# Optimization experiments

Hardware: AMD Instinct MI355X
Metric: run time of the kernel (lower is better)

The kernel has to match this reference:

```python
import jax, jax.numpy as jnp
import numpy as np

T, C, H = 4096, 1024, 16
D = C // H  # head dim = 64


def setup_inputs() -> dict:
    key = jax.random.key(0)
    k1, k2, k3 = jax.random.split(key, 3)
    x = jax.random.normal(k1, (T, C), dtype=jnp.float32)
    w_attn = jax.random.normal(k2, (C, 3 * C), dtype=jnp.float32) * (1.0 / np.sqrt(C))
    w_proj = jax.random.normal(k3, (C, C), dtype=jnp.float32) * (1.0 / np.sqrt(C))
    return {"x": x, "w_attn": w_attn, "w_proj": w_proj, "num_frames": 64}


def reference(x, w_attn, w_proj, num_frames):
    t, c = x.shape
    d = c // H
    qkv = x @ w_attn                       # (T, 3C)
    q, k, v = jnp.split(qkv, 3, axis=-1)   # each (T, C)
    # (T, H, D) -> (H, T, D)
    q = q.reshape(t, H, d).transpose(1, 0, 2)
    k = k.reshape(t, H, d).transpose(1, 0, 2)
    v = v.reshape(t, H, d).transpose(1, 0, 2)
    # causal mask with dense global prefix: every query may attend to the
    # first num_frames keys in addition to the causal lower triangle.
    rows = jnp.arange(t)[:, None]
    cols = jnp.arange(t)[None, :]
    mask = (cols <= rows) | (cols < num_frames)   # (T, T) bool
    scores = jnp.einsum('htd,hsd->hts', q, k) * (1.0 / np.sqrt(d))  # (H,T,T)
    scores = jnp.where(mask[None], scores, jnp.float32(-jnp.inf))
    att = jax.nn.softmax(scores, axis=-1)
    y = jnp.einsum('hts,hsd->htd', att, v)        # (H, T, D)
    y = y.transpose(1, 0, 2).reshape(t, c)        # (T, C)
    return y @ w_proj
```

## Files before the change

kernel.cpp:

```cpp
#include <hip/hip_runtime.h>
#include <hip/hip_bf16.h>

#define Tq 4096
#define Cdim 1024
#define NH 16
#define DH 64

typedef __attribute__((ext_vector_type(8))) short short8;
typedef __attribute__((ext_vector_type(4))) float f32x4;

#define SCLQ 0.1803368801111204f

__device__ __forceinline__ unsigned short f2bf(float f) {
  union { float f; unsigned int u; } v; v.f = f;
  unsigned int r = v.u + 0x7FFFu + ((v.u >> 16) & 1u);
  return (unsigned short)(r >> 16);
}

__device__ __forceinline__ float bf2f(unsigned short u) {
  union { unsigned int u; float f; } v; v.u = ((unsigned int)u) << 16;
  return v.f;
}

__device__ __forceinline__ unsigned int cvtpk_bf16(float lo, float hi) {
  unsigned int r;
  asm volatile("v_cvt_pk_bf16_f32 %0, %1, %2" : "=v"(r) : "v"(lo), "v"(hi));
  return r;
}

__global__ void cvt_kernel(const float* __restrict__ in, unsigned short* __restrict__ out, int n) {
  int idx = (blockIdx.x * blockDim.x + threadIdx.x) * 4;
  if (idx + 3 < n) {
    float4 v = *reinterpret_cast<const float4*>(in + idx);
    ushort4 o;
    o.x = f2bf(v.x); o.y = f2bf(v.y); o.z = f2bf(v.z); o.w = f2bf(v.w);
    *reinterpret_cast<ushort4*>(out + idx) = o;
  }
}

__global__ void transpose_cvt(const float* __restrict__ in, unsigned short* __restrict__ out,
                              int R, int Ccols) {
  __shared__ float tile[64][65];
  int c0 = blockIdx.x * 64, r0 = blockIdx.y * 64;
  int tx = threadIdx.x & 63;
  int ty = threadIdx.x >> 6;
  #pragma unroll
  for (int rr = 0; rr < 64; rr += 4)
    tile[rr + ty][tx] = in[(r0 + rr + ty) * Ccols + c0 + tx];
  __syncthreads();
  #pragma unroll
  for (int rr = 0; rr < 64; rr += 4)
    out[(c0 + rr + ty) * R + r0 + tx] = f2bf(tile[tx][rr + ty]);
}

template<int OUT_MODE>
__global__ __launch_bounds__(256, 3)
void gemm_bt(const unsigned short* __restrict__ A,
             const unsigned short* __restrict__ B,
             void* __restrict__ Cout,
             int M, int N, int K)
{
  __shared__ __align__(16) unsigned short As[128][64];
  __shared__ __align__(16) unsigned short Bs[128][64];
  const int tid = threadIdx.x;
  const int lane = tid & 63;
  const int wave = tid >> 6;
  const int wm = wave >> 1, wn = wave & 1;

  const int chunk = gridDim.x >> 3;
  const int b = blockIdx.x;
  const int swz = (b & 7) * chunk + (b >> 3);
  const int n0 = (swz >> 5) * 128;
  const int m0 = (swz & 31) * 128;

  f32x4 acc[4][4] = {};

  const int lrow = lane >> 3;
  const int lcol = (lane & 7) * 8;

  for (int k0 = 0; k0 < K; k0 += 64) {
    __syncthreads();
    #pragma unroll
    for (int t = 0; t < 4; ++t) {
      const int r = wave * 32 + t * 8;
      __builtin_amdgcn_global_load_lds(
        (const __attribute__((address_space(1))) void*)&A[(size_t)(m0 + r + lrow) * K + k0 + lcol],
        (__attribute__((address_space(3))) void*)&As[r][0], 16, 0, 0);
      __builtin_amdgcn_global_load_lds(
        (const __attribute__((address_space(1))) void*)&B[(size_t)(n0 + r + lrow) * K + k0 + lcol],
        (__attribute__((address_space(3))) void*)&Bs[r][0], 16, 0, 0);
    }
    __syncthreads();
    #pragma unroll
    for (int kk = 0; kk < 64; kk += 32) {
      const int frow = lane & 15;
      const int fcol = kk + 8 * (lane >> 4);
      short8 a[4], bfr[4];
      #pragma unroll
      for (int i = 0; i < 4; ++i) {
        a[i]   = *reinterpret_cast<const short8*>(&As[wm * 64 + i * 16 + frow][fcol]);
        bfr[i] = *reinterpret_cast<const short8*>(&Bs[wn * 64 + i * 16 + frow][fcol]);
      }
      #pragma unroll
      for (int i = 0; i < 4; ++i)
        #pragma unroll
        for (int j = 0; j < 4; ++j)
          acc[i][j] = __builtin_amdgcn_mfma_f32_16x16x32_bf16(a[i], bfr[j], acc[i][j], 0, 0, 0);
    }
  }

  const int rbase = (lane >> 4) * 4;
  const int ccol = lane & 15;
  #pragma unroll
  for (int i = 0; i < 4; ++i) {
    const int row0 = m0 + wm * 64 + i * 16 + rbase;
    #pragma unroll
    for (int j = 0; j < 4; ++j) {
      const int col = n0 + wn * 64 + j * 16 + ccol;
      if (OUT_MODE == 0) {
        unsigned short* q = (unsigned short*)Cout;
        int sec = col >> 10, rem = col & 1023;
        int hh = rem >> 6, d = rem & 63;
        if (sec == 2) {
          ushort4 pk;
          pk.x = f2bf(acc[i][j][0]); pk.y = f2bf(acc[i][j][1]);
          pk.z = f2bf(acc[i][j][2]); pk.w = f2bf(acc[i][j][3]);
          *reinterpret_cast<ushort4*>(
              &q[((size_t)(2 * NH + hh) * DH + d) * Tq + row0]) = pk;
        } else {
          const float mult = (sec == 0) ? SCLQ : 1.0f;
          #pragma unroll
          for (int r = 0; r < 4; ++r)
            q[(((size_t)sec * NH + hh) * Tq + row0 + r) * DH + d] = f2bf(acc[i][j][r] * mult);
        }
      } else {
        #pragma unroll
        for (int r = 0; r < 4; ++r)
          ((float*)Cout)[(row0 + r) * N + col] = acc[i][j][r];
      }
    }
  }
}

__global__ __launch_bounds__(256, 4)
void attn_kernel(const unsigned short* __restrict__ qkv,
                 unsigned short* __restrict__ po01,
                 unsigned short* __restrict__ po2,
                 float* __restrict__ pl,
                 const int* __restrict__ nf_ptr)
{
  __shared__ __align__(16) unsigned short Ks[128][72];
  __shared__ __align__(16) unsigned short VTs[64][136];

  const int tid  = threadIdx.x;
  const int lane = tid & 63;
  const int w    = tid >> 6;
  const int g    = lane >> 4;
  const int li   = lane & 15;

  const int h   = blockIdx.x & 15;
  const int bb  = blockIdx.x >> 4;
  const int s   = bb % 3;
  const int qc  = 63 - bb / 3;
  const int q0  = qc * 64;
  const int nf  = nf_ptr[0];

  const unsigned short* Qh  = qkv + (size_t)h * Tq * DH;
  const unsigned short* Kh  = qkv + (size_t)(NH + h) * Tq * DH;
  const unsigned short* VTh = qkv + (size_t)(2 * NH + h) * DH * Tq;

  const int qrow = q0 + w * 16 + li;
  short8 qf[2];
  #pragma unroll
  for (int kk = 0; kk < 2; ++kk)
    qf[kk] = *reinterpret_cast<const short8*>(&Qh[qrow * DH + kk * 32 + 8 * g]);

  f32x4 o[4] = {};
  f32x4 ol = {};

  short8 ones;
  #pragma unroll
  for (int e = 0; e < 8; ++e) ones[e] = (short)0x3F80;

  int lastt = q0 + 63;
  if (nf - 1 > lastt) lastt = nf - 1;
  const int T = (lastt >> 7) + 1;

  const int krow0 = tid >> 3;
  const int kcol  = (tid & 7) * 8;
  const int vrow0 = tid >> 4;
  const int vcol  = (tid & 15) * 8;

  {
    const int nx = s * 128;
    short8 nk[4], nv[4];
    #pragma unroll
    for (int j = 0; j < 4; ++j) {
      nk[j] = *reinterpret_cast<const short8*>(&Kh[(nx + krow0 + 32 * j) * DH + kcol]);
      nv[j] = *reinterpret_cast<const short8*>(&VTh[(size_t)(vrow0 + 16 * j) * Tq + nx + vcol]);
    }
    #pragma unroll
    for (int j = 0; j < 4; ++j) {
      *reinterpret_cast<short8*>(&Ks[krow0 + 32 * j][kcol]) = nk[j];
      *reinterpret_cast<short8*>(&VTs[vrow0 + 16 * j][vcol]) = nv[j];
    }
  }
  __syncthreads();

  for (int t = s; t < T; t += 3) {
    const int kv0 = t * 128;
    const bool havenext = (t + 3 < T);
    short8 nk[4], nv[4];
    if (havenext) {
      const int nx = kv0 + 384;
      #pragma unroll
      for (int j = 0; j < 4; ++j) {
        nk[j] = *reinterpret_cast<const short8*>(&Kh[(nx + krow0 + 32 * j) * DH + kcol]);
        nv[j] = *reinterpret_cast<const short8*>(&VTh[(size_t)(vrow0 + 16 * j) * Tq + nx + vcol]);
      }
    }

    #pragma unroll
    for (int h2 = 0; h2 < 2; ++h2) {
      const int kvb = kv0 + h2 * 64;

      f32x4 sarr[4];
      __builtin_amdgcn_s_setprio(1);
      #pragma unroll
      for (int nb = 0; nb < 4; ++nb) {
        f32x4 a = {};
        #pragma unroll
        for (int kk = 0; kk < 2; ++kk) {
          short8 kf = *reinterpret_cast<const short8*>(
              &Ks[h2 * 64 + nb * 16 + li][kk * 32 + 8 * g]);
          a = __builtin_amdgcn_mfma_f32_16x16x32_bf16(kf, qf[kk], a, 0, 0, 0);
        }
        sarr[nb] = a;
      }
      __builtin_amdgcn_s_setprio(0);

      const bool needmask = !((kvb + 63 <= q0 + w * 16) || (kvb + 63 < nf));
      float p[4][4];
      #pragma unroll
      for (int nb = 0; nb < 4; ++nb) {
        #pragma unroll
        for (int r = 0; r < 4; ++r) {
          float v = sarr[nb][r];
          if (needmask) {
            const int kvi = kvb + nb * 16 + 4 * g + r;
            if (!(kvi <= qrow || kvi < nf)) v = -1e30f;
          }
          p[nb][r] = exp2f(v);
        }
      }

      #pragma unroll
      for (int kk = 0; kk < 2; ++kk) {
        unsigned int X1 = cvtpk_bf16(p[2 * kk][0], p[2 * kk][1]);
        unsigned int X2 = cvtpk_bf16(p[2 * kk][2], p[2 * kk][3]);
        unsigned int Y1 = cvtpk_bf16(p[2 * kk + 1][0], p[2 * kk + 1][1]);
        unsigned int Y2 = cvtpk_bf16(p[2 * kk + 1][2], p[2 * kk + 1][3]);
        asm volatile("v_permlane32_swap_b32 %0, %1" : "+v"(X1), "+v"(Y1));
        asm volatile("v_permlane32_swap_b32 %0, %1" : "+v"(X2), "+v"(Y2));
        asm volatile("v_permlane16_swap_b32 %0, %1" : "+v"(X1), "+v"(Y1));
        asm volatile("v_permlane16_swap_b32 %0, %1" : "+v"(X2), "+v"(Y2));
        union { unsigned int u[4]; short8 s8; } W;
        W.u[0] = X1; W.u[1] = X2; W.u[2] = Y1; W.u[3] = Y2;
        __builtin_amdgcn_s_setprio(1);
        #pragma unroll
        for (int db = 0; db < 4; ++db) {
          short8 vb = *reinterpret_cast<const short8*>(
              &VTs[db * 16 + li][h2 * 64 + kk * 32 + 8 * g]);
          o[db] = __builtin_amdgcn_mfma_f32_16x16x32_bf16(vb, W.s8, o[db], 0, 0, 0);
        }
        ol = __builtin_amdgcn_mfma_f32_16x16x32_bf16(ones, W.s8, ol, 0, 0, 0);
        __builtin_amdgcn_s_setprio(0);
      }
    }

    if (havenext) {
      __syncthreads();
      #pragma unroll
      for (int j = 0; j < 4; ++j) {
        *reinterpret_cast<short8*>(&Ks[krow0 + 32 * j][kcol]) = nk[j];
        *reinterpret_cast<short8*>(&VTs[vrow0 + 16 * j][vcol]) = nv[j];
      }
      __syncthreads();
    }
  }

  unsigned short* pp = (s == 2 ? po2 : po01 + (size_t)s * NH * Tq * DH)
                       + ((size_t)h * Tq + qrow) * DH;
  #pragma unroll
  for (int db = 0; db < 4; ++db) {
    ushort4 pk;
    pk.x = f2bf(o[db][0]);
    pk.y = f2bf(o[db][1]);
    pk.z = f2bf(o[db][2]);
    pk.w = f2bf(o[db][3]);
    *reinterpret_cast<ushort4*>(&pp[db * 16 + 4 * g]) = pk;
  }
  if (g == 0)
    pl[((size_t)s * NH + h) * Tq + qrow] = ol[0];
}

__global__ __launch_bounds__(256)
void merge_kernel(const unsigned short* __restrict__ po01,
                  const unsigned short* __restrict__ po2,
                  const float* __restrict__ pl,
                  unsigned short* __restrict__ ybf)
{
  const int idx = blockIdx.x * 256 + threadIdx.x;
  const int d8  = idx & 7;
  const int row = (idx >> 3) & 4095;
  const int h   = idx >> 15;
  const size_t base = ((size_t)h * Tq + row) * DH + d8 * 8;
  short8 a = *reinterpret_cast<const short8*>(&po01[base]);
  short8 b = *reinterpret_cast<const short8*>(&po01[(size_t)NH * Tq * DH + base]);
  short8 c = *reinterpret_cast<const short8*>(&po2[base]);
  const float l0 = pl[(size_t)h * Tq + row];
  const float l1 = pl[((size_t)NH + h) * Tq + row];
  const float l2 = pl[((size_t)2 * NH + h) * Tq + row];
  const float inv = 1.0f / (l0 + l1 + l2);
  short8 outv;
  #pragma unroll
  for (int j = 0; j < 8; ++j) {
    float v = (bf2f((unsigned short)a[j]) + bf2f((unsigned short)b[j])
               + bf2f((unsigned short)c[j])) * inv;
    outv[j] = (short)f2bf(v);
  }
  *reinterpret_cast<short8*>(&ybf[(size_t)row * Cdim + h * DH + d8 * 8]) = outv;
}

extern "C" void kernel_launch(void* const* d_in, const int* in_sizes, int n_in,
                              void* d_out, int out_size, void* d_ws, size_t ws_size,
                              hipStream_t stream) {
  (void)in_sizes; (void)n_in; (void)out_size; (void)ws_size;
  const float* x  = (const float*)d_in[0];
  const float* wa = (const float*)d_in[1];
  const float* wp = (const float*)d_in[2];
  const int*   nf = (const int*)d_in[3];
  float* out = (float*)d_out;

  char* ws = (char*)d_ws;
  unsigned short* x_bf = (unsigned short*)(ws);
  unsigned short* waT  = (unsigned short*)(ws + (size_t)8  * 1024 * 1024);
  unsigned short* wpT  = (unsigned short*)(ws + (size_t)14 * 1024 * 1024);
  unsigned short* qkvb = (unsigned short*)(ws + (size_t)16 * 1024 * 1024);
  unsigned short* ybf  = (unsigned short*)(ws + (size_t)40 * 1024 * 1024);

  unsigned short* po01 = (unsigned short*)d_out;
  float* pl = (float*)(ws);
  unsigned short* po2 = (unsigned short*)(ws + (size_t)1 * 1024 * 1024);

  cvt_kernel<<<4096, 256, 0, stream>>>(x, x_bf, Tq * Cdim);
  transpose_cvt<<<dim3(48, 16), 256, 0, stream>>>(wa, waT, 1024, 3072);
  transpose_cvt<<<dim3(16, 16), 256, 0, stream>>>(wp, wpT, 1024, 1024);
  gemm_bt<0><<<768, 256, 0, stream>>>(x_bf, waT, (void*)qkvb, Tq, 3 * Cdim, Cdim);
  attn_kernel<<<3072, 256, 0, stream>>>(qkvb, po01, po2, pl, nf);
  merge_kernel<<<2048, 256, 0, stream>>>(po01, po2, pl, ybf);
  gemm_bt<1><<<256, 256, 0, stream>>>(ybf, wpT, (void*)out, Tq, Cdim, Cdim);
}
```

Baseline: 150.0 us.

## Load K/V MFMA fragments directly from global memory, dropping LDS staging

The attention kernel no longer stages K and V^T tiles through shared memory with a register prefetch and double barrier. Each wave now loads its MFMA operand fragments straight from global memory (relying on L1/L2 to share them across the 4 waves) and keeps only a lightweight s_barrier per iteration to keep waves roughly in step. This removes LDS traffic and __syncthreads stalls, but each wave issues its own redundant global loads and the software prefetch of the next tile is gone, so load latency may be exposed.

```diff
diff --git a/kernel.cpp b/kernel.cpp
--- a/kernel.cpp
+++ b/kernel.cpp
@@ -149,9 +149,6 @@
                  float* __restrict__ pl,
                  const int* __restrict__ nf_ptr)
 {
-  __shared__ __align__(16) unsigned short Ks[128][72];
-  __shared__ __align__(16) unsigned short VTs[64][136];
-
   const int tid  = threadIdx.x;
   const int lane = tid & 63;
   const int w    = tid >> 6;
@@ -186,43 +183,29 @@
   if (nf - 1 > lastt) lastt = nf - 1;
   const int T = (lastt >> 7) + 1;
 
-  const int krow0 = tid >> 3;
-  const int kcol  = (tid & 7) * 8;
-  const int vrow0 = tid >> 4;
-  const int vcol  = (tid & 15) * 8;
-
-  {
-    const int nx = s * 128;
-    short8 nk[4], nv[4];
-    #pragma unroll
-    for (int j = 0; j < 4; ++j) {
-      nk[j] = *reinterpret_cast<const short8*>(&Kh[(nx + krow0 + 32 * j) * DH + kcol]);
-      nv[j] = *reinterpret_cast<const short8*>(&VTh[(size_t)(vrow0 + 16 * j) * Tq + nx + vcol]);
-    }
-    #pragma unroll
-    for (int j = 0; j < 4; ++j) {
-      *reinterpret_cast<short8*>(&Ks[krow0 + 32 * j][kcol]) = nk[j];
-      *reinterpret_cast<short8*>(&VTs[vrow0 + 16 * j][vcol]) = nv[j];
-    }
-  }
-  __syncthreads();
+  const int kfo = li * DH + 8 * g;
+  const size_t vfo = (size_t)li * Tq + 8 * g;
 
   for (int t = s; t < T; t += 3) {
     const int kv0 = t * 128;
-    const bool havenext = (t + 3 < T);
-    short8 nk[4], nv[4];
-    if (havenext) {
-      const int nx = kv0 + 384;
-      #pragma unroll
-      for (int j = 0; j < 4; ++j) {
-        nk[j] = *reinterpret_cast<const short8*>(&Kh[(nx + krow0 + 32 * j) * DH + kcol]);
-        nv[j] = *reinterpret_cast<const short8*>(&VTh[(size_t)(vrow0 + 16 * j) * Tq + nx + vcol]);
-      }
-    }
 
     #pragma unroll
     for (int h2 = 0; h2 < 2; ++h2) {
       const int kvb = kv0 + h2 * 64;
+      const unsigned short* kb = Kh + (size_t)kvb * DH + kfo;
+      const unsigned short* vbp = VTh + vfo + kvb;
+
+      short8 kf[4][2], vv[4][2];
+      #pragma unroll
+      for (int nb = 0; nb < 4; ++nb)
+        #pragma unroll
+        for (int kk = 0; kk < 2; ++kk)
+          kf[nb][kk] = *reinterpret_cast<const short8*>(&kb[nb * 16 * DH + kk * 32]);
+      #pragma unroll
+      for (int db = 0; db < 4; ++db)
+        #pragma unroll
+        for (int kk = 0; kk < 2; ++kk)
+          vv[db][kk] = *reinterpret_cast<const short8*>(&vbp[(size_t)db * 16 * Tq + kk * 32]);
 
       f32x4 sarr[4];
       __builtin_amdgcn_s_setprio(1);
@@ -230,11 +213,8 @@
       for (int nb = 0; nb < 4; ++nb) {
         f32x4 a = {};
         #pragma unroll
-        for (int kk = 0; kk < 2; ++kk) {
-          short8 kf = *reinterpret_cast<const short8*>(
-              &Ks[h2 * 64 + nb * 16 + li][kk * 32 + 8 * g]);
-          a = __builtin_amdgcn_mfma_f32_16x16x32_bf16(kf, qf[kk], a, 0, 0, 0);
-        }
+        for (int kk = 0; kk < 2; ++kk)
+          a = __builtin_amdgcn_mfma_f32_16x16x32_bf16(kf[nb][kk], qf[kk], a, 0, 0, 0);
         sarr[nb] = a;
       }
       __builtin_amdgcn_s_setprio(0);
@@ -268,25 +248,14 @@
         W.u[0] = X1; W.u[1] = X2; W.u[2] = Y1; W.u[3] = Y2;
         __builtin_amdgcn_s_setprio(1);
         #pragma unroll
-        for (int db = 0; db < 4; ++db) {
-          short8 vb = *reinterpret_cast<const short8*>(
-              &VTs[db * 16 + li][h2 * 64 + kk * 32 + 8 * g]);
-          o[db] = __builtin_amdgcn_mfma_f32_16x16x32_bf16(vb, W.s8, o[db], 0, 0, 0);
-        }
+        for (int db = 0; db < 4; ++db)
+          o[db] = __builtin_amdgcn_mfma_f32_16x16x32_bf16(vv[db][kk], W.s8, o[db], 0, 0, 0);
         ol = __builtin_amdgcn_mfma_f32_16x16x32_bf16(ones, W.s8, ol, 0, 0, 0);
         __builtin_amdgcn_s_setprio(0);
       }
     }
 
-    if (havenext) {
-      __syncthreads();
-      #pragma unroll
-      for (int j = 0; j < 4; ++j) {
-        *reinterpret_cast<short8*>(&Ks[krow0 + 32 * j][kcol]) = nk[j];
-        *reinterpret_cast<short8*>(&VTs[vrow0 + 16 * j][vcol]) = nv[j];
-      }
-      __syncthreads();
-    }
+    __builtin_amdgcn_s_barrier();
   }
 
   unsigned short* pp = (s == 2 ? po2 : po01 + (size_t)s * NH * Tq * DH)
```

Result: slower. 326.7 us (+117.7%).

## Process 128 query rows per attention block, reusing K/V fragments across two row tiles

Applied to the files above, without the earlier changes.

Each attention workgroup now covers 128 query rows instead of 64, and each wave handles two 16-row sub-tiles. K fragments are loaded from LDS once and reused for both sub-tiles, and V fragments are shared across both PV MFMAs, halving LDS reads and global K/V staging per query. The grid shrinks from 3072 to 1536 blocks. The cost is more register pressure (two sets of accumulators and Q fragments), fewer blocks to hide latency, and coarser causal tiles, which means some extra masked work near the diagonal.

```diff
diff --git a/kernel.cpp b/kernel.cpp
--- a/kernel.cpp
+++ b/kernel.cpp
@@ -161,28 +161,33 @@
   const int h   = blockIdx.x & 15;
   const int bb  = blockIdx.x >> 4;
   const int s   = bb % 3;
-  const int qc  = 63 - bb / 3;
-  const int q0  = qc * 64;
+  const int qc  = 31 - bb / 3;
+  const int q0  = qc * 128;
   const int nf  = nf_ptr[0];
 
   const unsigned short* Qh  = qkv + (size_t)h * Tq * DH;
   const unsigned short* Kh  = qkv + (size_t)(NH + h) * Tq * DH;
   const unsigned short* VTh = qkv + (size_t)(2 * NH + h) * DH * Tq;
 
-  const int qrow = q0 + w * 16 + li;
-  short8 qf[2];
-  #pragma unroll
-  for (int kk = 0; kk < 2; ++kk)
-    qf[kk] = *reinterpret_cast<const short8*>(&Qh[qrow * DH + kk * 32 + 8 * g]);
-
-  f32x4 o[4] = {};
-  f32x4 ol = {};
+  int qrow[2];
+  qrow[0] = q0 + w * 32 + li;
+  qrow[1] = qrow[0] + 16;
+  short8 qf[2][2];
+  #pragma unroll
+  for (int r0 = 0; r0 < 2; ++r0)
+    #pragma unroll
+    for (int kk = 0; kk < 2; ++kk)
+      qf[r0][kk] = *reinterpret_cast<const short8*>(
+          &Qh[qrow[r0] * DH + kk * 32 + 8 * g]);
+
+  f32x4 o[2][4] = {};
+  f32x4 ol[2] = {};
 
   short8 ones;
   #pragma unroll
   for (int e = 0; e < 8; ++e) ones[e] = (short)0x3F80;
 
-  int lastt = q0 + 63;
+  int lastt = q0 + 127;
   if (nf - 1 > lastt) lastt = nf - 1;
   const int T = (lastt >> 7) + 1;
 
@@ -224,58 +229,77 @@
     for (int h2 = 0; h2 < 2; ++h2) {
       const int kvb = kv0 + h2 * 64;
 
-      f32x4 sarr[4];
+      short8 kf[4][2];
+      #pragma unroll
+      for (int nb = 0; nb < 4; ++nb)
+        #pragma unroll
+        for (int kk = 0; kk < 2; ++kk)
+          kf[nb][kk] = *reinterpret_cast<const short8*>(
+              &Ks[h2 * 64 + nb * 16 + li][kk * 32 + 8 * g]);
+
+      short8 W[2][2];
+
+      #pragma unroll
+      for (int r0 = 0; r0 < 2; ++r0) {
+        f32x4 sarr[4];
+        __builtin_amdgcn_s_setprio(1);
+        #pragma unroll
+        for (int nb = 0; nb < 4; ++nb) {
+          f32x4 a = {};
+          #pragma unroll
+          for (int kk = 0; kk < 2; ++kk)
+            a = __builtin_amdgcn_mfma_f32_16x16x32_bf16(kf[nb][kk], qf[r0][kk], a, 0, 0, 0);
+          sarr[nb] = a;
+        }
+        __builtin_amdgcn_s_setprio(0);
+
+        const bool needmask = !((kvb + 63 <= q0 + w * 32 + r0 * 16) || (kvb + 63 < nf));
+        float p[4][4];
+        #pragma unroll
+        for (int nb = 0; nb < 4; ++nb) {
+          #pragma unroll
+          for (int r = 0; r < 4; ++r) {
+            float v = sarr[nb][r];
+            if (needmask) {
+              const int kvi = kvb + nb * 16 + 4 * g + r;
+              if (!(kvi <= qrow[r0] || kvi < nf)) v = -1e30f;
+            }
+            p[nb][r] = exp2f(v);
+          }
+        }
+
+        #pragma unroll
+        for (int kk = 0; kk < 2; ++kk) {
+          unsigned int X1 = cvtpk_bf16(p[2 * kk][0], p[2 * kk][1]);
+          unsigned int X2 = cvtpk_bf16(p[2 * kk][2], p[2 * kk][3]);
+          unsigned int Y1 = cvtpk_bf16(p[2 * kk + 1][0], p[2 * kk + 1][1]);
+          unsigned int Y2 = cvtpk_bf16(p[2 * kk + 1][2], p[2 * kk + 1][3]);
+          asm volatile("v_permlane32_swap_b32 %0, %1" : "+v"(X1), "+v"(Y1));
+          asm volatile("v_permlane32_swap_b32 %0, %1" : "+v"(X2), "+v"(Y2));
+          asm volatile("v_permlane16_swap_b32 %0, %1" : "+v"(X1), "+v"(Y1));
+          asm volatile("v_permlane16_swap_b32 %0, %1" : "+v"(X2), "+v"(Y2));
+          union { unsigned int u[4]; short8 s8; } Wt;
+          Wt.u[0] = X1; Wt.u[1] = X2; Wt.u[2] = Y1; Wt.u[3] = Y2;
+          W[r0][kk] = Wt.s8;
+        }
+      }
+
       __builtin_amdgcn_s_setprio(1);
       #pragma unroll
-      for (int nb = 0; nb < 4; ++nb) {
-        f32x4 a = {};
-        #pragma unroll
-        for (int kk = 0; kk < 2; ++kk) {
-          short8 kf = *reinterpret_cast<const short8*>(
-              &Ks[h2 * 64 + nb * 16 + li][kk * 32 + 8 * g]);
-          a = __builtin_amdgcn_mfma_f32_16x16x32_bf16(kf, qf[kk], a, 0, 0, 0);
-        }
-        sarr[nb] = a;
-      }
-      __builtin_amdgcn_s_setprio(0);
-
-      const bool needmask = !((kvb + 63 <= q0 + w * 16) || (kvb + 63 < nf));
-      float p[4][4];
-      #pragma unroll
-      for (int nb = 0; nb < 4; ++nb) {
-        #pragma unroll
-        for (int r = 0; r < 4; ++r) {
-          float v = sarr[nb][r];
-          if (needmask) {
-            const int kvi = kvb + nb * 16 + 4 * g + r;
-            if (!(kvi <= qrow || kvi < nf)) v = -1e30f;
-          }
-          p[nb][r] = exp2f(v);
-        }
-      }
-
-      #pragma unroll
       for (int kk = 0; kk < 2; ++kk) {
-        unsigned int X1 = cvtpk_bf16(p[2 * kk][0], p[2 * kk][1]);
-        unsigned int X2 = cvtpk_bf16(p[2 * kk][2], p[2 * kk][3]);
-        unsigned int Y1 = cvtpk_bf16(p[2 * kk + 1][0], p[2 * kk + 1][1]);
-        unsigned int Y2 = cvtpk_bf16(p[2 * kk + 1][2], p[2 * kk + 1][3]);
-        asm volatile("v_permlane32_swap_b32 %0, %1" : "+v"(X1), "+v"(Y1));
-        asm volatile("v_permlane32_swap_b32 %0, %1" : "+v"(X2), "+v"(Y2));
-        asm volatile("v_permlane16_swap_b32 %0, %1" : "+v"(X1), "+v"(Y1));
-        asm volatile("v_permlane16_swap_b32 %0, %1" : "+v"(X2), "+v"(Y2));
-        union { unsigned int u[4]; short8 s8; } W;
-        W.u[0] = X1; W.u[1] = X2; W.u[2] = Y1; W.u[3] = Y2;
-        __builtin_amdgcn_s_setprio(1);
         #pragma unroll
         for (int db = 0; db < 4; ++db) {
           short8 vb = *reinterpret_cast<const short8*>(
               &VTs[db * 16 + li][h2 * 64 + kk * 32 + 8 * g]);
-          o[db] = __builtin_amdgcn_mfma_f32_16x16x32_bf16(vb, W.s8, o[db], 0, 0, 0);
-        }
-        ol = __builtin_amdgcn_mfma_f32_16x16x32_bf16(ones, W.s8, ol, 0, 0, 0);
-        __builtin_amdgcn_s_setprio(0);
-      }
+          #pragma unroll
+          for (int r0 = 0; r0 < 2; ++r0)
+            o[r0][db] = __builtin_amdgcn_mfma_f32_16x16x32_bf16(vb, W[r0][kk], o[r0][db], 0, 0, 0);
+        }
+        #pragma unroll
+        for (int r0 = 0; r0 < 2; ++r0)
+          ol[r0] = __builtin_amdgcn_mfma_f32_16x16x32_bf16(ones, W[r0][kk], ol[r0], 0, 0, 0);
+      }
+      __builtin_amdgcn_s_setprio(0);
     }
 
     if (havenext) {
@@ -289,19 +313,22 @@
     }
   }
 
-  unsigned short* pp = (s == 2 ? po2 : po01 + (size_t)s * NH * Tq * DH)
-                       + ((size_t)h * Tq + qrow) * DH;
-  #pragma unroll
-  for (int db = 0; db < 4; ++db) {
-    ushort4 pk;
-    pk.x = f2bf(o[db][0]);
-    pk.y = f2bf(o[db][1]);
-    pk.z = f2bf(o[db][2]);
-    pk.w = f2bf(o[db][3]);
-    *reinterpret_cast<ushort4*>(&pp[db * 16 + 4 * g]) = pk;
-  }
-  if (g == 0)
-    pl[((size_t)s * NH + h) * Tq + qrow] = ol[0];
+  #pragma unroll
+  for (int r0 = 0; r0 < 2; ++r0) {
+    unsigned short* pp = (s == 2 ? po2 : po01 + (size_t)s * NH * Tq * DH)
+                         + ((size_t)h * Tq + qrow[r0]) * DH;
+    #pragma unroll
+    for (int db = 0; db < 4; ++db) {
+      ushort4 pk;
+      pk.x = f2bf(o[r0][db][0]);
+      pk.y = f2bf(o[r0][db][1]);
+      pk.z = f2bf(o[r0][db][2]);
+      pk.w = f2bf(o[r0][db][3]);
+      *reinterpret_cast<ushort4*>(&pp[db * 16 + 4 * g]) = pk;
+    }
+    if (g == 0)
+      pl[((size_t)s * NH + h) * Tq + qrow[r0]] = ol[r0][0];
+  }
 }
 
 __global__ __launch_bounds__(256)
@@ -357,7 +384,7 @@
   transpose_cvt<<<dim3(48, 16), 256, 0, stream>>>(wa, waT, 1024, 3072);
   transpose_cvt<<<dim3(16, 16), 256, 0, stream>>>(wp, wpT, 1024, 1024);
   gemm_bt<0><<<768, 256, 0, stream>>>(x_bf, waT, (void*)qkvb, Tq, 3 * Cdim, Cdim);
-  attn_kernel<<<3072, 256, 0, stream>>>(qkvb, po01, po2, pl, nf);
+  attn_kernel<<<1536, 256, 0, stream>>>(qkvb, po01, po2, pl, nf);
   merge_kernel<<<2048, 256, 0, stream>>>(po01, po2, pl, ybf);
   gemm_bt<1><<<256, 256, 0, stream>>>(ybf, wpT, (void*)out, Tq, Cdim, Cdim);
 }
```

Result: slower. 214.8 us (+43.1%).
